# Kernel optimization log

Measured on AMD Instinct MI355X. Metric: run time of the kernel, lower is better.

Reference implementation:

```python
import jax, jax.numpy as jnp
import numpy as np

B, M, N, HID, H, P = 16, 1024, 1024, 512, 8, 2
DH = HID // H


def setup_inputs() -> dict:
    key = jax.random.key(0)
    k1, k2, k3, k4 = jax.random.split(key, 4)
    X = jax.random.normal(k1, (B, M, HID), dtype=jnp.float32)
    Y = jax.random.normal(k2, (B, N, HID), dtype=jnp.float32)
    # learned pad prefixes (kaiming-uniform in torch; any init is fine for a numerics baseline)
    bound = np.sqrt(1.0 / HID)
    pad_x = jax.random.uniform(k3, (P, HID), dtype=jnp.float32, minval=-bound, maxval=bound)
    pad_y = jax.random.uniform(k4, (P, HID), dtype=jnp.float32, minval=-bound, maxval=bound)
    return {"X": X, "Y": Y, "pad_x": pad_x, "pad_y": pad_y}


def _project(T, pad):
    # prepend learned pad rows, split into heads -> [B, H, L+P, DH]
    b = T.shape[0]
    T = jnp.concatenate([jnp.broadcast_to(pad[None], (b, P, HID)), T], axis=1)
    return T.reshape(b, T.shape[1], H, DH).transpose(0, 2, 1, 3)


def reference(X, Y, pad_x, pad_y):
    Xp = _project(X, pad_x)  # [B,H,Mp,DH], query=key=value
    Yp = _project(Y, pad_y)  # [B,H,Np,DH]
    # shared similarity matrix (no 1/sqrt(d) scaling in the original)
    sim = jnp.einsum('bhmd,bhnd->bhmn', Xp, Yp)  # [B,H,Mp,Np]
    # masks in the original are all-ones (pad rows + torch.ones), so masked_fill is a no-op
    attn_X_by_Y = jax.nn.softmax(sim, axis=2)  # softmax over Mp (rows)
    attn_Y_by_X = jax.nn.softmax(sim, axis=3)  # softmax over Np (cols)
    # X attends in Y: attn^T @ X_value -> [B,H,Np,DH]
    X_in_Y = jnp.einsum('bhmn,bhmd->bhnd', attn_X_by_Y, Xp)[:, :, P:, :]
    X_in_Y = X_in_Y.transpose(0, 2, 1, 3).reshape(X.shape[0], -1, HID)  # [B,N,HID]
    # Y attends in X: attn @ Y_value -> [B,H,Mp,DH]
    Y_in_X = jnp.einsum('bhmn,bhnd->bhmd', attn_Y_by_X, Yp)[:, :, P:, :]
    Y_in_X = Y_in_X.transpose(0, 2, 1, 3).reshape(Y.shape[0], -1, HID)  # [B,M,HID]
    return X_in_Y, Y_in_X
```

## Files before the change

kernel.cpp:

```cpp
#include <hip/hip_runtime.h>
#include <hip/hip_bf16.h>
#include <stdint.h>

typedef _Float16 f16x8_t __attribute__((ext_vector_type(8)));
typedef float    f32x4_t __attribute__((ext_vector_type(4)));
typedef short    s16x8_t __attribute__((ext_vector_type(8)));
typedef unsigned int u32;

#define MFMA16 __builtin_amdgcn_mfma_f32_16x16x32_f16

#if __has_builtin(__builtin_amdgcn_exp2f)
#define EXP2(x) __builtin_amdgcn_exp2f(x)
#else
#define EXP2(x) exp2f(x)
#endif

__device__ __forceinline__ u32 PKRTZ(float a, float b) {
    return __builtin_bit_cast(u32, __builtin_amdgcn_cvt_pkrtz(a, b));
}

constexpr int Bb   = 16;
constexpr int HIDc = 512;
constexpr int DHc  = 64;
constexpr int SEQc = 1024;

constexpr int QT = 128;
constexpr int KT = 64;
constexpr int NTILES = SEQc / KT;

constexpr float LOG2E_F = 1.4426950408889634f;
constexpr float DTHR    = 11.5f;

constexpr int ROWB    = 144;
constexpr int K_BASE  = 0;
constexpr int VT_BASE = 64 * ROWB;
constexpr int P_BASE  = VT_BASE + 80 * ROWB;
constexpr int P_WAVE  = 16 * ROWB;
constexpr int LDS_TOTAL = P_BASE + 4 * P_WAVE;

__global__ __launch_bounds__(256, 4)
void xattn_kernel(const float* __restrict__ X, const float* __restrict__ Y,
                  const float* __restrict__ padx, const float* __restrict__ pady,
                  float* __restrict__ out)
{
    __shared__ __align__(16) unsigned char pool[LDS_TOTAL];

    const int tid  = threadIdx.x;
    const int w    = tid >> 6;
    const int lane = tid & 63;
    const int g    = lane >> 4;
    const int q16  = lane & 15;

    const unsigned hid = blockIdx.x + gridDim.x * (blockIdx.y + gridDim.y * blockIdx.z);
    const unsigned lid = (hid & 7u) * 256u + (hid >> 3);
    const int qt   = lid & 7;
    const int bh   = (lid >> 3) & 127;
    const int pass = lid >> 10;
    const int b    = bh >> 3;
    const int h    = bh & 7;

    const float* Qp   = pass == 0 ? X : Y;
    const float* KVp  = pass == 0 ? Y : X;
    const float* padp = pass == 0 ? pady : padx;
    float* outp = out + (pass == 0 ? (size_t)Bb * SEQc * HIDc : (size_t)0);

    f16x8_t qf[2][2];
#pragma unroll
    for (int sub = 0; sub < 2; ++sub) {
        const float* qrow = Qp + ((size_t)b * SEQc + qt * QT + w * 32 + sub * 16 + q16) * HIDc + h * DHc;
#pragma unroll
        for (int s = 0; s < 2; ++s) {
            const float* src = qrow + s * 32 + g * 8;
            float4 a = *(const float4*)src;
            float4 c = *(const float4*)(src + 4);
            u32 p0 = PKRTZ(a.x * LOG2E_F, a.y * LOG2E_F);
            u32 p1 = PKRTZ(a.z * LOG2E_F, a.w * LOG2E_F);
            u32 p2 = PKRTZ(c.x * LOG2E_F, c.y * LOG2E_F);
            u32 p3 = PKRTZ(c.z * LOG2E_F, c.w * LOG2E_F);
            uint4 uu = {p0, p1, p2, p3};
            qf[sub][s] = __builtin_bit_cast(f16x8_t, uu);
        }
    }

    const float* padh = padp + h * DHc;
    float m0r, m1r;
    f32x4_t Oacc0[4], Oacc1[4], lext0, lext1;
    {
#pragma unroll
        for (int sub = 0; sub < 2; ++sub) {
            float s0 = 0.f, s1 = 0.f;
#pragma unroll
            for (int s = 0; s < 2; ++s)
#pragma unroll
                for (int j = 0; j < 8; ++j) {
                    float qv = (float)qf[sub][s][j];
                    int d = s * 32 + g * 8 + j;
                    s0 += qv * padh[d];
                    s1 += qv * padh[HIDc + d];
                }
            s0 += __shfl_xor(s0, 16); s0 += __shfl_xor(s0, 32);
            s1 += __shfl_xor(s1, 16); s1 += __shfl_xor(s1, 32);
            float m = fmaxf(s0, s1);
            float e0 = EXP2(s0 - m), e1 = EXP2(s1 - m);
            f32x4_t* Oa = sub ? Oacc1 : Oacc0;
#pragma unroll
            for (int db = 0; db < 4; ++db)
#pragma unroll
                for (int i = 0; i < 4; ++i) {
                    int d = db * 16 + g * 4 + i;
                    Oa[db][i] = e0 * padh[d] + e1 * padh[HIDc + d];
                }
            f32x4_t le = {0.f, 0.f, 0.f, 0.f};
            le[0] = (g == 0) ? (e0 + e1) : 0.f;
            if (sub) { lext1 = le; m1r = m; } else { lext0 = le; m0r = m; }
        }
    }

    unsigned vaddr[2][5];
#pragma unroll
    for (int t = 0; t < 2; ++t)
#pragma unroll
        for (int db = 0; db < 5; ++db) {
            int row = db * 16 + q16;
            int sw  = (db * 2 + (q16 >> 3)) & 7;
            vaddr[t][db] = (unsigned)(VT_BASE + row * ROWB + (((t * 4 + g) ^ sw) << 4));
        }
    const unsigned kb0 = (unsigned)(K_BASE + q16 * ROWB + g * 16);
    const unsigned pwb = (unsigned)(P_BASE + w * P_WAVE + q16 * ROWB + g * 8);
    const unsigned prb = (unsigned)(P_BASE + w * P_WAVE + q16 * ROWB + g * 16);

    const int tr = tid >> 3, tc = tid & 7;
    const float* ksrc = KVp + ((size_t)b * SEQc + 2 * tr) * HIDc + h * DHc + tc * 8;
    const unsigned kwb  = (unsigned)(K_BASE + (2 * tr) * ROWB + tc * 16);
    const unsigned vtwb = (unsigned)(VT_BASE + (tc * 8) * ROWB + (((tr >> 2) ^ tc) << 4) + (tr & 3) * 4);

#pragma unroll
    for (int it = 0; it < 2; ++it) {
        int idx = tid + it * 256;
        int row = 64 + (idx >> 5);
        int wd  = idx & 31;
        u32 val = (row == 64) ? 0x3C003C00u : 0u;
        unsigned a = (unsigned)(VT_BASE + row * ROWB + (((wd >> 2) ^ ((row >> 3) & 7)) << 4) + (wd & 3) * 4);
        *(u32*)(pool + a) = val;
    }

    auto softmax_pv = [&](f32x4_t (&sacc)[4], f32x4_t (&Oacc)[4], f32x4_t& lext, float& mrun) {
        float pmax = fmaxf(fmaxf(fmaxf(sacc[0][0], sacc[0][1]), fmaxf(sacc[0][2], sacc[0][3])),
                           fmaxf(fmaxf(sacc[1][0], sacc[1][1]), fmaxf(sacc[1][2], sacc[1][3])));
        float pmax2 = fmaxf(fmaxf(fmaxf(sacc[2][0], sacc[2][1]), fmaxf(sacc[2][2], sacc[2][3])),
                            fmaxf(fmaxf(sacc[3][0], sacc[3][1]), fmaxf(sacc[3][2], sacc[3][3])));
        pmax = fmaxf(pmax, pmax2);
        pmax = fmaxf(pmax, __shfl_xor(pmax, 16));
        pmax = fmaxf(pmax, __shfl_xor(pmax, 32));
        if (!__all(pmax <= mrun + DTHR)) {
            float mnew = fmaxf(mrun, pmax);
            float corr = EXP2(mrun - mnew);
            mrun = mnew;
#pragma unroll
            for (int db = 0; db < 4; ++db)
#pragma unroll
                for (int i = 0; i < 4; ++i) Oacc[db][i] *= corr;
            lext[0] *= corr;
        }
        const float m = mrun;
#pragma unroll
        for (int nb = 0; nb < 4; ++nb) {
            u32 w0 = PKRTZ(EXP2(sacc[nb][0] - m), EXP2(sacc[nb][1] - m));
            u32 w1 = PKRTZ(EXP2(sacc[nb][2] - m), EXP2(sacc[nb][3] - m));
            uint2 pk = {w0, w1};
            *(uint2*)(pool + pwb + nb * 32) = pk;
        }
        asm volatile("" ::: "memory");
        __builtin_amdgcn_s_setprio(1);
#pragma unroll
        for (int t = 0; t < 2; ++t) {
            f16x8_t pb = __builtin_bit_cast(f16x8_t, *(const s16x8_t*)(pool + prb + t * 64));
#pragma unroll
            for (int db = 0; db < 4; ++db) {
                s16x8_t va = *(const s16x8_t*)(pool + vaddr[t][db]);
                Oacc[db] = MFMA16(__builtin_bit_cast(f16x8_t, va), pb, Oacc[db], 0, 0, 0);
            }
            s16x8_t v1 = *(const s16x8_t*)(pool + vaddr[t][4]);
            lext = MFMA16(__builtin_bit_cast(f16x8_t, v1), pb, lext, 0, 0, 0);
        }
        __builtin_amdgcn_s_setprio(0);
    };

    for (int kt = 0; kt < NTILES; ++kt) {
        __syncthreads();
        {
            const float* srow = ksrc + (size_t)kt * KT * HIDc;
            float4 a0 = *(const float4*)srow;
            float4 a1 = *(const float4*)(srow + 4);
            float4 c0 = *(const float4*)(srow + HIDc);
            float4 c1 = *(const float4*)(srow + HIDc + 4);
            uint4 k0 = {PKRTZ(a0.x, a0.y), PKRTZ(a0.z, a0.w), PKRTZ(a1.x, a1.y), PKRTZ(a1.z, a1.w)};
            uint4 k1 = {PKRTZ(c0.x, c0.y), PKRTZ(c0.z, c0.w), PKRTZ(c1.x, c1.y), PKRTZ(c1.z, c1.w)};
            *(uint4*)(pool + kwb) = k0;
            *(uint4*)(pool + kwb + ROWB) = k1;
            float fa[8] = {a0.x, a0.y, a0.z, a0.w, a1.x, a1.y, a1.z, a1.w};
            float fc[8] = {c0.x, c0.y, c0.z, c0.w, c1.x, c1.y, c1.z, c1.w};
#pragma unroll
            for (int j = 0; j < 8; ++j)
                *(u32*)(pool + vtwb + j * ROWB) = PKRTZ(fa[j], fc[j]);
        }
        __syncthreads();

        {
            f32x4_t sacc0[4], sacc1[4];
#pragma unroll
            for (int nb = 0; nb < 4; ++nb) {
                sacc0[nb] = f32x4_t{0.f, 0.f, 0.f, 0.f};
                sacc1[nb] = f32x4_t{0.f, 0.f, 0.f, 0.f};
            }
            __builtin_amdgcn_s_setprio(1);
#pragma unroll
            for (int s = 0; s < 2; ++s)
#pragma unroll
                for (int nb = 0; nb < 4; ++nb) {
                    s16x8_t kh = *(const s16x8_t*)(pool + kb0 + nb * (16 * ROWB) + s * 64);
                    f16x8_t kf = __builtin_bit_cast(f16x8_t, kh);
                    sacc0[nb] = MFMA16(kf, qf[0][s], sacc0[nb], 0, 0, 0);
                    sacc1[nb] = MFMA16(kf, qf[1][s], sacc1[nb], 0, 0, 0);
                }
            __builtin_amdgcn_s_setprio(0);
            softmax_pv(sacc0, Oacc0, lext0, m0r);
            softmax_pv(sacc1, Oacc1, lext1, m1r);
        }
    }

    float lv0 = __shfl(lext0[0], q16);
    float lv1 = __shfl(lext1[0], q16);
    const float inv[2] = {1.0f / lv0, 1.0f / lv1};
    float* fp = (float*)pool;
    const int r = tid >> 2, c = tid & 3;
#pragma unroll
    for (int sub = 0; sub < 2; ++sub) {
        __syncthreads();
        const f32x4_t* Oa = sub ? Oacc1 : Oacc0;
#pragma unroll
        for (int db = 0; db < 4; ++db)
#pragma unroll
            for (int i = 0; i < 4; ++i)
                fp[(w * 16 + q16) * 68 + db * 16 + g * 4 + i] = Oa[db][i] * inv[sub];
        __syncthreads();
        const int grow = qt * QT + (r >> 4) * 32 + sub * 16 + (r & 15);
        float* dst = outp + ((size_t)b * SEQc + grow) * HIDc + h * DHc + c * 16;
        const float* srcp = fp + r * 68 + c * 16;
#pragma unroll
        for (int k = 0; k < 4; ++k)
            *(float4*)(dst + k * 4) = *(const float4*)(srcp + k * 4);
    }
}

extern "C" void kernel_launch(void* const* d_in, const int* in_sizes, int n_in,
                              void* d_out, int out_size, void* d_ws, size_t ws_size,
                              hipStream_t stream) {
    const float* X    = (const float*)d_in[0];
    const float* Y    = (const float*)d_in[1];
    const float* padx = (const float*)d_in[2];
    const float* pady = (const float*)d_in[3];
    float* out = (float*)d_out;
    (void)in_sizes; (void)n_in; (void)out_size; (void)d_ws; (void)ws_size;

    dim3 grid(SEQc / QT, Bb * 8, 2);
    hipLaunchKernelGGL(xattn_kernel, grid, dim3(256), 0, stream, X, Y, padx, pady, out);
}
```

Measured before the change: 120.3 us.

## Double-buffer K/V tiles in LDS and prefetch the next tile during compute

Splits the K/V staging area into two LDS buffers and issues the global loads for the next tile before computing on the current one, writing them to the alternate buffer afterwards. This removes one barrier per tile and hides global load latency behind the MFMA and softmax work. In exchange, LDS use grows and launch bounds drop from 4 to 3 blocks per CU, which reduces occupancy and adds register pressure from holding prefetched values across the compute phase.

Measured after the change: 123.8 us. 1.03x slower.

```diff
diff --git a/kernel.cpp b/kernel.cpp
--- a/kernel.cpp
+++ b/kernel.cpp
@@ -32,13 +32,13 @@
 constexpr float DTHR    = 11.5f;
 
 constexpr int ROWB    = 144;
-constexpr int K_BASE  = 0;
-constexpr int VT_BASE = 64 * ROWB;
-constexpr int P_BASE  = VT_BASE + 80 * ROWB;
-constexpr int P_WAVE  = 16 * ROWB;
-constexpr int LDS_TOTAL = P_BASE + 4 * P_WAVE;
-
-__global__ __launch_bounds__(256, 4)
+constexpr int VT_OFF     = 64 * ROWB;
+constexpr int BUF_STRIDE = VT_OFF + 80 * ROWB;
+constexpr int P_BASE     = 2 * BUF_STRIDE;
+constexpr int P_WAVE     = 16 * ROWB;
+constexpr int LDS_TOTAL  = P_BASE + 4 * P_WAVE;
+
+__global__ __launch_bounds__(256, 3)
 void xattn_kernel(const float* __restrict__ X, const float* __restrict__ Y,
                   const float* __restrict__ padx, const float* __restrict__ pady,
                   float* __restrict__ out)
@@ -123,28 +123,49 @@
         for (int db = 0; db < 5; ++db) {
             int row = db * 16 + q16;
             int sw  = (db * 2 + (q16 >> 3)) & 7;
-            vaddr[t][db] = (unsigned)(VT_BASE + row * ROWB + (((t * 4 + g) ^ sw) << 4));
-        }
-    const unsigned kb0 = (unsigned)(K_BASE + q16 * ROWB + g * 16);
+            vaddr[t][db] = (unsigned)(VT_OFF + row * ROWB + (((t * 4 + g) ^ sw) << 4));
+        }
+    const unsigned kb0 = (unsigned)(q16 * ROWB + g * 16);
     const unsigned pwb = (unsigned)(P_BASE + w * P_WAVE + q16 * ROWB + g * 8);
     const unsigned prb = (unsigned)(P_BASE + w * P_WAVE + q16 * ROWB + g * 16);
 
     const int tr = tid >> 3, tc = tid & 7;
     const float* ksrc = KVp + ((size_t)b * SEQc + 2 * tr) * HIDc + h * DHc + tc * 8;
-    const unsigned kwb  = (unsigned)(K_BASE + (2 * tr) * ROWB + tc * 16);
-    const unsigned vtwb = (unsigned)(VT_BASE + (tc * 8) * ROWB + (((tr >> 2) ^ tc) << 4) + (tr & 3) * 4);
-
-#pragma unroll
-    for (int it = 0; it < 2; ++it) {
-        int idx = tid + it * 256;
-        int row = 64 + (idx >> 5);
-        int wd  = idx & 31;
-        u32 val = (row == 64) ? 0x3C003C00u : 0u;
-        unsigned a = (unsigned)(VT_BASE + row * ROWB + (((wd >> 2) ^ ((row >> 3) & 7)) << 4) + (wd & 3) * 4);
-        *(u32*)(pool + a) = val;
-    }
-
-    auto softmax_pv = [&](f32x4_t (&sacc)[4], f32x4_t (&Oacc)[4], f32x4_t& lext, float& mrun) {
+    const unsigned kwb  = (unsigned)((2 * tr) * ROWB + tc * 16);
+    const unsigned vtwb = (unsigned)(VT_OFF + (tc * 8) * ROWB + (((tr >> 2) ^ tc) << 4) + (tr & 3) * 4);
+
+#pragma unroll
+    for (int bb = 0; bb < 2; ++bb)
+#pragma unroll
+        for (int it = 0; it < 2; ++it) {
+            int idx = tid + it * 256;
+            int row = 64 + (idx >> 5);
+            int wd  = idx & 31;
+            u32 val = (row == 64) ? 0x3C003C00u : 0u;
+            unsigned a = (unsigned)(bb * BUF_STRIDE + VT_OFF + row * ROWB +
+                                    (((wd >> 2) ^ ((row >> 3) & 7)) << 4) + (wd & 3) * 4);
+            *(u32*)(pool + a) = val;
+        }
+
+    auto loadtile = [&](int idx, float4& a0, float4& a1, float4& c0, float4& c1) {
+        const float* srow = ksrc + (size_t)idx * KT * HIDc;
+        a0 = *(const float4*)srow;          a1 = *(const float4*)(srow + 4);
+        c0 = *(const float4*)(srow + HIDc); c1 = *(const float4*)(srow + HIDc + 4);
+    };
+    auto stage_write = [&](int bo, const float4& a0, const float4& a1,
+                           const float4& c0, const float4& c1) {
+        uint4 k0 = {PKRTZ(a0.x, a0.y), PKRTZ(a0.z, a0.w), PKRTZ(a1.x, a1.y), PKRTZ(a1.z, a1.w)};
+        uint4 k1 = {PKRTZ(c0.x, c0.y), PKRTZ(c0.z, c0.w), PKRTZ(c1.x, c1.y), PKRTZ(c1.z, c1.w)};
+        *(uint4*)(pool + bo + kwb) = k0;
+        *(uint4*)(pool + bo + kwb + ROWB) = k1;
+        float fa[8] = {a0.x, a0.y, a0.z, a0.w, a1.x, a1.y, a1.z, a1.w};
+        float fc[8] = {c0.x, c0.y, c0.z, c0.w, c1.x, c1.y, c1.z, c1.w};
+#pragma unroll
+        for (int j = 0; j < 8; ++j)
+            *(u32*)(pool + bo + vtwb + j * ROWB) = PKRTZ(fa[j], fc[j]);
+    };
+    auto softmax_pv = [&](int bo, f32x4_t (&sacc)[4], f32x4_t (&Oacc)[4],
+                          f32x4_t& lext, float& mrun) {
         float pmax = fmaxf(fmaxf(fmaxf(sacc[0][0], sacc[0][1]), fmaxf(sacc[0][2], sacc[0][3])),
                            fmaxf(fmaxf(sacc[1][0], sacc[1][1]), fmaxf(sacc[1][2], sacc[1][3])));
         float pmax2 = fmaxf(fmaxf(fmaxf(sacc[2][0], sacc[2][1]), fmaxf(sacc[2][2], sacc[2][3])),
@@ -177,55 +198,56 @@
             f16x8_t pb = __builtin_bit_cast(f16x8_t, *(const s16x8_t*)(pool + prb + t * 64));
 #pragma unroll
             for (int db = 0; db < 4; ++db) {
-                s16x8_t va = *(const s16x8_t*)(pool + vaddr[t][db]);
+                s16x8_t va = *(const s16x8_t*)(pool + bo + vaddr[t][db]);
                 Oacc[db] = MFMA16(__builtin_bit_cast(f16x8_t, va), pb, Oacc[db], 0, 0, 0);
             }
-            s16x8_t v1 = *(const s16x8_t*)(pool + vaddr[t][4]);
+            s16x8_t v1 = *(const s16x8_t*)(pool + bo + vaddr[t][4]);
             lext = MFMA16(__builtin_bit_cast(f16x8_t, v1), pb, lext, 0, 0, 0);
         }
         __builtin_amdgcn_s_setprio(0);
     };
-
-    for (int kt = 0; kt < NTILES; ++kt) {
-        __syncthreads();
+    auto compute = [&](int bo) {
+        f32x4_t sacc0[4], sacc1[4];
+#pragma unroll
+        for (int nb = 0; nb < 4; ++nb) {
+            sacc0[nb] = f32x4_t{0.f, 0.f, 0.f, 0.f};
+            sacc1[nb] = f32x4_t{0.f, 0.f, 0.f, 0.f};
+        }
+        __builtin_amdgcn_s_setprio(1);
+#pragma unroll
+        for (int s = 0; s < 2; ++s)
+#pragma unroll
+            for (int nb = 0; nb < 4; ++nb) {
+                s16x8_t kh = *(const s16x8_t*)(pool + bo + kb0 + nb * (16 * ROWB) + s * 64);
+                f16x8_t kf = __builtin_bit_cast(f16x8_t, kh);
+                sacc0[nb] = MFMA16(kf, qf[0][s], sacc0[nb], 0, 0, 0);
+                sacc1[nb] = MFMA16(kf, qf[1][s], sacc1[nb], 0, 0, 0);
+            }
+        __builtin_amdgcn_s_setprio(0);
+        softmax_pv(bo, sacc0, Oacc0, lext0, m0r);
+        softmax_pv(bo, sacc1, Oacc1, lext1, m1r);
+    };
+
+    {
+        float4 a0, a1, c0, c1;
+        loadtile(0, a0, a1, c0, c1);
+        stage_write(0, a0, a1, c0, c1);
+    }
+    __syncthreads();
+    for (int kt = 0; kt < NTILES; kt += 2) {
         {
-            const float* srow = ksrc + (size_t)kt * KT * HIDc;
-            float4 a0 = *(const float4*)srow;
-            float4 a1 = *(const float4*)(srow + 4);
-            float4 c0 = *(const float4*)(srow + HIDc);
-            float4 c1 = *(const float4*)(srow + HIDc + 4);
-            uint4 k0 = {PKRTZ(a0.x, a0.y), PKRTZ(a0.z, a0.w), PKRTZ(a1.x, a1.y), PKRTZ(a1.z, a1.w)};
-            uint4 k1 = {PKRTZ(c0.x, c0.y), PKRTZ(c0.z, c0.w), PKRTZ(c1.x, c1.y), PKRTZ(c1.z, c1.w)};
-            *(uint4*)(pool + kwb) = k0;
-            *(uint4*)(pool + kwb + ROWB) = k1;
-            float fa[8] = {a0.x, a0.y, a0.z, a0.w, a1.x, a1.y, a1.z, a1.w};
-            float fc[8] = {c0.x, c0.y, c0.z, c0.w, c1.x, c1.y, c1.z, c1.w};
-#pragma unroll
-            for (int j = 0; j < 8; ++j)
-                *(u32*)(pool + vtwb + j * ROWB) = PKRTZ(fa[j], fc[j]);
-        }
-        __syncthreads();
-
+            float4 a0, a1, c0, c1;
+            loadtile(kt + 1, a0, a1, c0, c1);
+            compute(0);
+            stage_write(BUF_STRIDE, a0, a1, c0, c1);
+            __syncthreads();
+        }
         {
-            f32x4_t sacc0[4], sacc1[4];
-#pragma unroll
-            for (int nb = 0; nb < 4; ++nb) {
-                sacc0[nb] = f32x4_t{0.f, 0.f, 0.f, 0.f};
-                sacc1[nb] = f32x4_t{0.f, 0.f, 0.f, 0.f};
-            }
-            __builtin_amdgcn_s_setprio(1);
-#pragma unroll
-            for (int s = 0; s < 2; ++s)
-#pragma unroll
-                for (int nb = 0; nb < 4; ++nb) {
-                    s16x8_t kh = *(const s16x8_t*)(pool + kb0 + nb * (16 * ROWB) + s * 64);
-                    f16x8_t kf = __builtin_bit_cast(f16x8_t, kh);
-                    sacc0[nb] = MFMA16(kf, qf[0][s], sacc0[nb], 0, 0, 0);
-                    sacc1[nb] = MFMA16(kf, qf[1][s], sacc1[nb], 0, 0, 0);
-                }
-            __builtin_amdgcn_s_setprio(0);
-            softmax_pv(sacc0, Oacc0, lext0, m0r);
-            softmax_pv(sacc1, Oacc1, lext1, m1r);
+            float4 a0, a1, c0, c1;
+            if (kt + 2 < NTILES) loadtile(kt + 2, a0, a1, c0, c1);
+            compute(BUF_STRIDE);
+            if (kt + 2 < NTILES) stage_write(0, a0, a1, c0, c1);
+            __syncthreads();
         }
     }
 
```
